# Performance work log

Measured on AMD Instinct MI355X. Metric: run time of the kernel, lower is better.

## Reference

```python
import jax, jax.numpy as jnp
import numpy as np

NUM_HEADS = 16
NUM_KV_HEADS = 4
ROPE_BASE = 10000.0
TRAIN_SEQ_LEN = 2048


def _rms_norm(x):
    eps = jnp.asarray(jnp.finfo(x.dtype).eps, x.dtype)
    return x * jax.lax.rsqrt(jnp.mean(x * x, axis=-1, keepdims=True) + eps)


def _rope_cos_sin(seq_len, head_dim, dtype):
    # seq_len <= TRAIN_SEQ_LEN -> no NTK rescaling, matches Rotary buffer path
    half = head_dim // 2
    inv_freq = 1.0 / (ROPE_BASE ** (jnp.arange(0, head_dim, 2, dtype=jnp.float32) / head_dim))
    t = jnp.arange(seq_len, dtype=jnp.float32)
    freqs = jnp.outer(t, inv_freq)  # [S, half]
    cos = jnp.cos(freqs)[None, :, None, :].astype(dtype)
    sin = jnp.sin(freqs)[None, :, None, :].astype(dtype)
    return cos, sin


def _apply_rotary(x, cos, sin):
    half = x.shape[-1] // 2
    x1, x2 = x[..., :half], x[..., half:]
    return jnp.concatenate([x1 * cos + x2 * sin, -x1 * sin + x2 * cos], axis=-1)


def setup_inputs() -> dict:
    key = jax.random.key(0)
    ks = jax.random.split(key, 5)
    B, S, D = 2, 2048, 2048
    kv_dim = NUM_KV_HEADS * (D // NUM_HEADS)
    sw = 0.02
    return {
        "x": jax.random.normal(ks[0], (B, S, D), jnp.float32),
        "Wq": jax.random.normal(ks[1], (D, D), jnp.float32) * sw,
        "Wk": jax.random.normal(ks[2], (kv_dim, D), jnp.float32) * sw,
        "Wv": jax.random.normal(ks[3], (kv_dim, D), jnp.float32) * sw,
        "Wproj": jax.random.normal(ks[4], (D, D), jnp.float32) * sw,
        "q_gain": jnp.ones((NUM_HEADS,), jnp.float32),
    }


def reference(x, Wq, Wk, Wv, Wproj, q_gain):
    B, S, D = x.shape
    H, Hkv = NUM_HEADS, NUM_KV_HEADS
    hd = D // H
    r = H // Hkv

    q = (x @ Wq.T).reshape(B, S, H, hd)
    k = (x @ Wk.T).reshape(B, S, Hkv, hd)
    v = (x @ Wv.T).reshape(B, S, Hkv, hd)

    q = _rms_norm(q)
    k = _rms_norm(k)

    cos, sin = _rope_cos_sin(S, hd, q.dtype)
    q = _apply_rotary(q, cos, sin)
    k = _apply_rotary(k, cos, sin)
    q = q * q_gain.astype(q.dtype)[None, None, :, None]

    # GQA: repeat kv heads (repeat_interleave along head dim)
    k = jnp.repeat(k, r, axis=2)  # [B,S,H,hd]
    v = jnp.repeat(v, r, axis=2)

    scale = 1.0 / jnp.sqrt(jnp.asarray(hd, q.dtype))
    scores = jnp.einsum("bqhd,bkhd->bhqk", q, k) * scale
    causal = jnp.tril(jnp.ones((S, S), dtype=bool))
    scores = jnp.where(causal[None, None], scores, jnp.asarray(-jnp.inf, scores.dtype))
    attn = jax.nn.softmax(scores, axis=-1)
    y = jnp.einsum("bhqk,bkhd->bqhd", attn, v)

    return y.reshape(B, S, D) @ Wproj.T
```

## Files before the change

### kernel.cpp

```cpp
#include <hip/hip_runtime.h>

#define D_MODEL 2048
#define SEQ 2048
#define BATCH 2
#define NH 16
#define NKV 4
#define HD 128
#define KVD (NKV * HD)
#define QKVN (D_MODEL + 2 * KVD)
#define MROWS (BATCH * SEQ)

typedef __attribute__((ext_vector_type(8))) short short8;
typedef __attribute__((ext_vector_type(4))) float f32x4;

__device__ __forceinline__ unsigned short f2bf(float f) {
    union { float f; unsigned int u; } v; v.f = f;
    unsigned int r = (v.u + 0x7FFFu + ((v.u >> 16) & 1u)) >> 16;
    return (unsigned short)r;
}

__device__ __forceinline__ unsigned short f2bf_pos(float f) {
    union { float f; unsigned int u; } v; v.f = f;
    return (unsigned short)((v.u + 0x8000u) >> 16);
}

__device__ __forceinline__ float bf2f(unsigned short u) {
    union { float f; unsigned int i; } v; v.i = ((unsigned int)u) << 16;
    return v.f;
}

__device__ __forceinline__ void async16(const void* g, void* l) {
    __builtin_amdgcn_global_load_lds((const __attribute__((address_space(1))) void*)g,
                                     (__attribute__((address_space(3))) void*)l, 16, 0, 0);
}

__global__ __launch_bounds__(256) void cast_all(const float* __restrict__ x,
                                                const float* __restrict__ wq,
                                                const float* __restrict__ wk,
                                                const float* __restrict__ wv,
                                                const float* __restrict__ wp,
                                                unsigned short* __restrict__ xb,
                                                unsigned short* __restrict__ wqkv,
                                                unsigned short* __restrict__ wpb) {
    int i = blockIdx.x * 256 + threadIdx.x;
    const float4* s; ushort4* d; int j;
    if (i < 2097152)      { s = (const float4*)x;  d = (ushort4*)xb;             j = i; }
    else if (i < 3145728) { s = (const float4*)wq; d = (ushort4*)wqkv;           j = i - 2097152; }
    else if (i < 3407872) { s = (const float4*)wk; d = (ushort4*)wqkv + 1048576; j = i - 3145728; }
    else if (i < 3670016) { s = (const float4*)wv; d = (ushort4*)wqkv + 1310720; j = i - 3407872; }
    else                  { s = (const float4*)wp; d = (ushort4*)wpb;            j = i - 3670016; }
    float4 v = s[j];
    ushort4 o;
    o.x = f2bf(v.x); o.y = f2bf(v.y); o.z = f2bf(v.z); o.w = f2bf(v.w);
    d[j] = o;
}

template <bool BF16OUT>
__global__ __launch_bounds__(256) void gemm_bt(const unsigned short* __restrict__ A,
                                               const unsigned short* __restrict__ W,
                                               void* __restrict__ Cv, int M, int N, int K) {
    __shared__ unsigned short As[128 * 32];
    __shared__ unsigned short Bs[128 * 32];
    const int tid  = threadIdx.x;
    const int lane = tid & 63;
    const int wave = tid >> 6;
    const int qm   = lane & 15;
    const int quad = lane >> 4;
    const int m0 = blockIdx.y * 128;
    const int n0 = blockIdx.x * 128;
    const int wm = (wave >> 1) * 64;
    const int wn = (wave & 1) * 64;

    f32x4 acc[4][4];
#pragma unroll
    for (int i = 0; i < 4; i++)
#pragma unroll
        for (int j = 0; j < 4; j++) acc[i][j] = (f32x4){0.f, 0.f, 0.f, 0.f};

    const int r1 = tid >> 2;
    const int c1 = (((tid & 3) ^ ((r1 >> 1) & 3)) * 8);
    const unsigned short* Ag = A + (size_t)(m0 + r1) * K + c1;
    const unsigned short* Wg = W + (size_t)(n0 + r1) * K + c1;
    unsigned short* AsW = &As[wave * 512];
    unsigned short* BsW = &Bs[wave * 512];
    const int swq = ((qm >> 1) & 3) * 8;

    for (int kt = 0; kt < K; kt += 32) {
        async16(Ag,                  AsW);
        async16(Ag + (size_t)64 * K, AsW + 2048);
        async16(Wg,                  BsW);
        async16(Wg + (size_t)64 * K, BsW + 2048);
        Ag += 32; Wg += 32;
        __syncthreads();
        short8 af[4], bfr[4];
#pragma unroll
        for (int mi = 0; mi < 4; mi++)
            af[mi] = *(const short8*)&As[(wm + mi * 16 + qm) * 32 + (quad * 8 ^ swq)];
#pragma unroll
        for (int ni = 0; ni < 4; ni++)
            bfr[ni] = *(const short8*)&Bs[(wn + ni * 16 + qm) * 32 + (quad * 8 ^ swq)];
#pragma unroll
        for (int mi = 0; mi < 4; mi++)
#pragma unroll
            for (int ni = 0; ni < 4; ni++)
                acc[mi][ni] = __builtin_amdgcn_mfma_f32_16x16x32_bf16(af[mi], bfr[ni], acc[mi][ni], 0, 0, 0);
        __syncthreads();
    }
#pragma unroll
    for (int mi = 0; mi < 4; mi++) {
#pragma unroll
        for (int r = 0; r < 4; r++) {
            int row = m0 + wm + mi * 16 + quad * 4 + r;
            if (BF16OUT) {
                unsigned short* Crow = (unsigned short*)Cv + (size_t)row * N + n0 + wn + qm;
#pragma unroll
                for (int ni = 0; ni < 4; ni++) Crow[ni * 16] = f2bf(acc[mi][ni][r]);
            } else {
                float* Crow = (float*)Cv + (size_t)row * N + n0 + wn + qm;
#pragma unroll
                for (int ni = 0; ni < 4; ni++) Crow[ni * 16] = acc[mi][ni][r];
            }
        }
    }
}

__global__ __launch_bounds__(256) void postproc(const unsigned short* __restrict__ qkvb,
                                                const float* __restrict__ gain,
                                                unsigned short* __restrict__ qb,
                                                unsigned short* __restrict__ kb) {
    const int m = blockIdx.x;
    const int b = m >> 11;
    const int s = m & 2047;
    const int wave = threadIdx.x >> 6;
    const int lane = threadIdx.x & 63;
    const unsigned short* row = qkvb + (size_t)m * QKVN;
    float inv_freq = __builtin_amdgcn_exp2f(-(float)lane * 0.20761871f);
    float ang = (float)s * inv_freq;
    float sn, cs;
    sincosf(ang, &sn, &cs);
    const float scale = 0.12751744f;
    for (int u = wave; u < 20; u += 4) {
        int off = (u < 16) ? (u * HD) : (D_MODEL + (u - 16) * HD);
        float x1 = bf2f(row[off + lane]);
        float x2 = bf2f(row[off + 64 + lane]);
        float ss = x1 * x1 + x2 * x2;
        ss += __shfl_xor(ss, 1);  ss += __shfl_xor(ss, 2);  ss += __shfl_xor(ss, 4);
        ss += __shfl_xor(ss, 8);  ss += __shfl_xor(ss, 16); ss += __shfl_xor(ss, 32);
        float rs = rsqrtf(ss * (1.0f / 128.0f) + 1.1920929e-07f);
        float a1 = x1 * rs, a2 = x2 * rs;
        float o1 = a1 * cs + a2 * sn;
        float o2 = -a1 * sn + a2 * cs;
        if (u < 16) {
            float g = gain[u] * scale;
            o1 *= g; o2 *= g;
            size_t base = ((size_t)(b * NH + u) * SEQ + s) * HD;
            qb[base + lane] = f2bf(o1);
            qb[base + 64 + lane] = f2bf(o2);
        } else {
            size_t base = ((size_t)(b * NKV + (u - 16)) * SEQ + s) * HD;
            kb[base + lane] = f2bf(o1);
            kb[base + 64 + lane] = f2bf(o2);
        }
    }
}

__global__ __launch_bounds__(256) void vtrans(const unsigned short* __restrict__ qkvb,
                                              unsigned short* __restrict__ vt) {
    __shared__ unsigned short tile[64][68];
    int idx = blockIdx.x;
    int st = idx & 31;
    int dt = (idx >> 5) & 1;
    int hk = (idx >> 6) & 3;
    int b  = idx >> 8;
    int t  = threadIdx.x;
    int cr = t >> 4;
    int cc = (t & 15) * 4;
#pragma unroll
    for (int j = 0; j < 4; j++) {
        int row = j * 16 + cr;
        const unsigned short* src = qkvb + (size_t)(b * SEQ + st * 64 + row) * QKVN
                                  + (D_MODEL + KVD) + hk * HD + dt * 64 + cc;
        *(ushort4*)&tile[row][cc] = *(const ushort4*)src;
    }
    __syncthreads();
#pragma unroll
    for (int j = 0; j < 4; j++) {
        int drow = j * 16 + cr;
        ushort4 ov;
        ov.x = tile[cc + 0][drow];
        ov.y = tile[cc + 1][drow];
        ov.z = tile[cc + 2][drow];
        ov.w = tile[cc + 3][drow];
        *(ushort4*)(vt + (size_t)((b * NKV + hk) * HD + dt * 64 + drow) * SEQ + st * 64 + cc) = ov;
    }
}

__global__ __launch_bounds__(256, 4) void attn(const unsigned short* __restrict__ qb,
                                               const unsigned short* __restrict__ kb,
                                               const unsigned short* __restrict__ vt,
                                               const float* __restrict__ gain,
                                               unsigned short* __restrict__ y) {
    __shared__ unsigned short Ks[4096];
    __shared__ unsigned short Vs[4096];
    __shared__ unsigned short plds[4][640];
    const int tid  = threadIdx.x;
    const int lane = tid & 63;
    const int wave = tid >> 6;
    const int bh   = blockIdx.x & 31;
    const int g  = blockIdx.x >> 5;
    const int gg = g & 7;
    const int gs = g >> 3;
    const int qt64 = (gs == 0) ? gg : (gs == 1) ? (31 - gg) : (gs == 2) ? (8 + gg) : (23 - gg);
    const int h = bh & 15;
    const int b = bh >> 4;
    const int qm   = lane & 15;
    const int quad = lane >> 4;
    const int q0    = qt64 * 64;
    const int qrow0 = q0 + wave * 16;
    const float M = 17.0f * fabsf(gain[h]);

    const unsigned short* Qp = qb + (((size_t)(b * NH + h)) * SEQ + qrow0) * HD;
    const unsigned short* Kp = kb + ((size_t)(b * NKV + (h >> 2))) * SEQ * HD;
    const unsigned short* Vp = vt + ((size_t)(b * NKV + (h >> 2))) * HD * SEQ;

    short8 qf[4];
#pragma unroll
    for (int c = 0; c < 4; c++)
        qf[c] = *(const short8*)(Qp + qm * HD + c * 32 + quad * 8);

    f32x4 o[8];
#pragma unroll
    for (int t = 0; t < 8; t++) o[t] = (f32x4){0.f, 0.f, 0.f, 0.f};
    float lr[4] = {0.f, 0.f, 0.f, 0.f};

    const int sr  = (tid & 127) >> 2;
    const int skc = ((tid & 3) ^ ((sr >> 1) & 3)) * 8;
    const unsigned short* KsA = Kp + sr * HD + (tid >> 7) * 32 + skc;
    const int vd  = tid >> 2;
    const int svc = ((tid & 3) ^ ((vd >> 1) & 3)) * 8;
    const unsigned short* VsA = Vp + (size_t)vd * SEQ + svc;
    char* KsB = (char*)Ks + wave * 1024;
    char* VsB = (char*)Vs + wave * 1024;
    unsigned short* P = &plds[wave][0];
    const int swq = ((qm >> 1) & 3) * 8;

    const int kvend = q0 + 64;
    for (int kv0 = 0; kv0 < kvend; kv0 += 32) {
        async16(KsA,            KsB);
        async16(KsA + 64,       KsB + 4096);
        async16(VsA,            VsB);
        async16(VsA + 64 * SEQ, VsB + 4096);
        KsA += 32 * HD;
        VsA += 32;
        __syncthreads();
        if (kv0 <= qrow0 + 15) {
            f32x4 s0 = (f32x4){0.f, 0.f, 0.f, 0.f};
            f32x4 s1 = (f32x4){0.f, 0.f, 0.f, 0.f};
#pragma unroll
            for (int c = 0; c < 4; c++) {
                short8 k0 = *(const short8*)&Ks[c * 1024 + qm * 32 + (quad * 8 ^ swq)];
                short8 k1 = *(const short8*)&Ks[c * 1024 + (16 + qm) * 32 + (quad * 8 ^ swq)];
                s0 = __builtin_amdgcn_mfma_f32_16x16x32_bf16(qf[c], k0, s0, 0, 0, 0);
                s1 = __builtin_amdgcn_mfma_f32_16x16x32_bf16(qf[c], k1, s1, 0, 0, 0);
            }
            if (kv0 + 31 > qrow0) {
#pragma unroll
                for (int r = 0; r < 4; r++) {
                    int qg = qrow0 + quad * 4 + r;
                    if (kv0 + qm > qg)      s0[r] = -3.0e38f;
                    if (kv0 + 16 + qm > qg) s1[r] = -3.0e38f;
                }
            }
            float p0[4], p1[4];
#pragma unroll
            for (int r = 0; r < 4; r++) {
                p0[r] = __builtin_amdgcn_exp2f(s0[r] - M);
                p1[r] = __builtin_amdgcn_exp2f(s1[r] - M);
                lr[r] += p0[r] + p1[r];
            }
#pragma unroll
            for (int r = 0; r < 4; r++) {
                P[(quad * 4 + r) * 40 + qm]      = f2bf_pos(p0[r]);
                P[(quad * 4 + r) * 40 + 16 + qm] = f2bf_pos(p1[r]);
            }
            short8 pa = *(const short8*)&P[qm * 40 + quad * 8];
#pragma unroll
            for (int t = 0; t < 8; t++) {
                short8 vf = *(const short8*)&Vs[(t * 16 + qm) * 32 + (quad * 8 ^ swq)];
                o[t] = __builtin_amdgcn_mfma_f32_16x16x32_bf16(pa, vf, o[t], 0, 0, 0);
            }
        }
        __syncthreads();
    }
    float rl[4];
#pragma unroll
    for (int r = 0; r < 4; r++) {
        float l = lr[r];
        l += __shfl_xor(l, 1);
        l += __shfl_xor(l, 2);
        l += __shfl_xor(l, 4);
        l += __shfl_xor(l, 8);
        rl[r] = 1.0f / l;
    }
#pragma unroll
    for (int t = 0; t < 8; t++) {
#pragma unroll
        for (int r = 0; r < 4; r++) {
            size_t row = (size_t)(b * SEQ + qrow0 + quad * 4 + r);
            y[row * D_MODEL + h * HD + t * 16 + qm] = f2bf(o[t][r] * rl[r]);
        }
    }
}

extern "C" void kernel_launch(void* const* d_in, const int* in_sizes, int n_in,
                              void* d_out, int out_size, void* d_ws, size_t ws_size,
                              hipStream_t stream) {
    const float* x  = (const float*)d_in[0];
    const float* Wq = (const float*)d_in[1];
    const float* Wk = (const float*)d_in[2];
    const float* Wv = (const float*)d_in[3];
    const float* Wp = (const float*)d_in[4];
    const float* qg = (const float*)d_in[5];

    char* ws = (char*)d_ws;
    unsigned short* xb   = (unsigned short*)(ws + 0);
    unsigned short* wqkv = (unsigned short*)(ws + 16777216);
    unsigned short* wp   = (unsigned short*)(ws + 29360128);
    unsigned short* qkvb = (unsigned short*)(ws + 37748736);
    unsigned short* qbuf = (unsigned short*)(ws + 88080384);
    unsigned short* kbuf = (unsigned short*)(ws + 104857600);
    unsigned short* vtb  = (unsigned short*)(ws + 109051904);
    unsigned short* y    = xb;

    cast_all<<<18432, 256, 0, stream>>>(x, Wq, Wk, Wv, Wp, xb, wqkv, wp);

    gemm_bt<true><<<dim3(24, 32), 256, 0, stream>>>(xb, wqkv, qkvb, MROWS, QKVN, D_MODEL);
    postproc<<<MROWS, 256, 0, stream>>>(qkvb, qg, qbuf, kbuf);
    vtrans<<<512, 256, 0, stream>>>(qkvb, vtb);
    attn<<<1024, 256, 0, stream>>>(qbuf, kbuf, vtb, qg, y);
    gemm_bt<false><<<dim3(16, 32), 256, 0, stream>>>(y, wp, (float*)d_out, MROWS, D_MODEL, D_MODEL);
}
```

Baseline: 319.0 us.

## Fuse QKV GEMM epilogue with RMSNorm/RoPE and V transpose; widen attention KV tile

Result: faster. 298.5 us (-6.4%).

```diff
diff --git a/kernel.cpp b/kernel.cpp
--- a/kernel.cpp
+++ b/kernel.cpp
@@ -55,10 +55,122 @@
     d[j] = o;
 }
 
-template <bool BF16OUT>
+__global__ __launch_bounds__(256) void gemm_qkv(const unsigned short* __restrict__ A,
+                                                const unsigned short* __restrict__ W,
+                                                const float* __restrict__ gain,
+                                                unsigned short* __restrict__ qbuf,
+                                                unsigned short* __restrict__ kbuf,
+                                                unsigned short* __restrict__ vtb) {
+    __shared__ unsigned short smem[128 * 137];
+    unsigned short* As = smem;
+    unsigned short* Bs = smem + 4096;
+    unsigned short* tile = smem;
+    const int K = D_MODEL;
+    const int tid  = threadIdx.x;
+    const int lane = tid & 63;
+    const int wave = tid >> 6;
+    const int qm   = lane & 15;
+    const int quad = lane >> 4;
+    const int m0 = blockIdx.y * 128;
+    const int bx = blockIdx.x;
+    const int n0 = bx * 128;
+    const int wm = (wave >> 1) * 64;
+    const int wn = (wave & 1) * 64;
+
+    f32x4 acc[4][4];
+#pragma unroll
+    for (int i = 0; i < 4; i++)
+#pragma unroll
+        for (int j = 0; j < 4; j++) acc[i][j] = (f32x4){0.f, 0.f, 0.f, 0.f};
+
+    const int r1 = tid >> 2;
+    const int c1 = (((tid & 3) ^ ((r1 >> 1) & 3)) * 8);
+    const unsigned short* Ag = A + (size_t)(m0 + r1) * K + c1;
+    const unsigned short* Wg = W + (size_t)(n0 + r1) * K + c1;
+    unsigned short* AsW = &As[wave * 512];
+    unsigned short* BsW = &Bs[wave * 512];
+    const int swq = ((qm >> 1) & 3) * 8;
+
+    for (int kt = 0; kt < K; kt += 32) {
+        async16(Ag,                  AsW);
+        async16(Ag + (size_t)64 * K, AsW + 2048);
+        async16(Wg,                  BsW);
+        async16(Wg + (size_t)64 * K, BsW + 2048);
+        Ag += 32; Wg += 32;
+        __syncthreads();
+        short8 af[4], bfr[4];
+#pragma unroll
+        for (int mi = 0; mi < 4; mi++)
+            af[mi] = *(const short8*)&As[(wm + mi * 16 + qm) * 32 + (quad * 8 ^ swq)];
+#pragma unroll
+        for (int ni = 0; ni < 4; ni++)
+            bfr[ni] = *(const short8*)&Bs[(wn + ni * 16 + qm) * 32 + (quad * 8 ^ swq)];
+#pragma unroll
+        for (int mi = 0; mi < 4; mi++)
+#pragma unroll
+            for (int ni = 0; ni < 4; ni++)
+                acc[mi][ni] = __builtin_amdgcn_mfma_f32_16x16x32_bf16(af[mi], bfr[ni], acc[mi][ni], 0, 0, 0);
+        __syncthreads();
+    }
+
+#pragma unroll
+    for (int mi = 0; mi < 4; mi++)
+#pragma unroll
+        for (int r = 0; r < 4; r++) {
+            int row = wm + mi * 16 + quad * 4 + r;
+#pragma unroll
+            for (int ni = 0; ni < 4; ni++)
+                tile[row * 137 + wn + ni * 16 + qm] = f2bf(acc[mi][ni][r]);
+        }
+    __syncthreads();
+
+    const int s_base = m0 & 2047;
+    const int bb = m0 >> 11;
+    if (bx < 20) {
+        const bool isq = bx < 16;
+        const float g = isq ? gain[bx] * 0.12751744f : 1.0f;
+        unsigned short* dst = isq
+            ? qbuf + ((size_t)(bb * NH + bx) * SEQ + s_base) * HD
+            : kbuf + ((size_t)(bb * NKV + (bx - 16)) * SEQ + s_base) * HD;
+        const float inv_freq = __builtin_amdgcn_exp2f(-(float)lane * 0.20761871f);
+        for (int rr = 0; rr < 32; rr++) {
+            int row = wave * 32 + rr;
+            float x1 = bf2f(tile[row * 137 + lane]);
+            float x2 = bf2f(tile[row * 137 + 64 + lane]);
+            float ss = x1 * x1 + x2 * x2;
+            ss += __shfl_xor(ss, 1);  ss += __shfl_xor(ss, 2);  ss += __shfl_xor(ss, 4);
+            ss += __shfl_xor(ss, 8);  ss += __shfl_xor(ss, 16); ss += __shfl_xor(ss, 32);
+            float rs = rsqrtf(ss * (1.0f / 128.0f) + 1.1920929e-07f);
+            float ang = (float)(s_base + row) * inv_freq;
+            float sn, cs;
+            sincosf(ang, &sn, &cs);
+            float a1 = x1 * rs, a2 = x2 * rs;
+            float o1 = (a1 * cs + a2 * sn) * g;
+            float o2 = (a2 * cs - a1 * sn) * g;
+            dst[(size_t)row * HD + lane]      = f2bf(o1);
+            dst[(size_t)row * HD + 64 + lane] = f2bf(o2);
+        }
+    } else {
+        const int hk = bx - 20;
+        unsigned short* dst = vtb + ((size_t)(bb * NKV + hk) * HD) * SEQ + s_base;
+        const int sc = (tid & 31) * 4;
+        const int d0 = tid >> 5;
+#pragma unroll
+        for (int i = 0; i < 16; i++) {
+            int d = d0 + 8 * i;
+            ushort4 ov;
+            ov.x = tile[(sc + 0) * 137 + d];
+            ov.y = tile[(sc + 1) * 137 + d];
+            ov.z = tile[(sc + 2) * 137 + d];
+            ov.w = tile[(sc + 3) * 137 + d];
+            *(ushort4*)(dst + (size_t)d * SEQ + sc) = ov;
+        }
+    }
+}
+
 __global__ __launch_bounds__(256) void gemm_bt(const unsigned short* __restrict__ A,
                                                const unsigned short* __restrict__ W,
-                                               void* __restrict__ Cv, int M, int N, int K) {
+                                               float* __restrict__ C, int M, int N, int K) {
     __shared__ unsigned short As[128 * 32];
     __shared__ unsigned short Bs[128 * 32];
     const int tid  = threadIdx.x;
@@ -111,87 +223,10 @@
 #pragma unroll
         for (int r = 0; r < 4; r++) {
             int row = m0 + wm + mi * 16 + quad * 4 + r;
-            if (BF16OUT) {
-                unsigned short* Crow = (unsigned short*)Cv + (size_t)row * N + n0 + wn + qm;
-#pragma unroll
-                for (int ni = 0; ni < 4; ni++) Crow[ni * 16] = f2bf(acc[mi][ni][r]);
-            } else {
-                float* Crow = (float*)Cv + (size_t)row * N + n0 + wn + qm;
-#pragma unroll
-                for (int ni = 0; ni < 4; ni++) Crow[ni * 16] = acc[mi][ni][r];
-            }
-        }
-    }
-}
-
-__global__ __launch_bounds__(256) void postproc(const unsigned short* __restrict__ qkvb,
-                                                const float* __restrict__ gain,
-                                                unsigned short* __restrict__ qb,
-                                                unsigned short* __restrict__ kb) {
-    const int m = blockIdx.x;
-    const int b = m >> 11;
-    const int s = m & 2047;
-    const int wave = threadIdx.x >> 6;
-    const int lane = threadIdx.x & 63;
-    const unsigned short* row = qkvb + (size_t)m * QKVN;
-    float inv_freq = __builtin_amdgcn_exp2f(-(float)lane * 0.20761871f);
-    float ang = (float)s * inv_freq;
-    float sn, cs;
-    sincosf(ang, &sn, &cs);
-    const float scale = 0.12751744f;
-    for (int u = wave; u < 20; u += 4) {
-        int off = (u < 16) ? (u * HD) : (D_MODEL + (u - 16) * HD);
-        float x1 = bf2f(row[off + lane]);
-        float x2 = bf2f(row[off + 64 + lane]);
-        float ss = x1 * x1 + x2 * x2;
-        ss += __shfl_xor(ss, 1);  ss += __shfl_xor(ss, 2);  ss += __shfl_xor(ss, 4);
-        ss += __shfl_xor(ss, 8);  ss += __shfl_xor(ss, 16); ss += __shfl_xor(ss, 32);
-        float rs = rsqrtf(ss * (1.0f / 128.0f) + 1.1920929e-07f);
-        float a1 = x1 * rs, a2 = x2 * rs;
-        float o1 = a1 * cs + a2 * sn;
-        float o2 = -a1 * sn + a2 * cs;
-        if (u < 16) {
-            float g = gain[u] * scale;
-            o1 *= g; o2 *= g;
-            size_t base = ((size_t)(b * NH + u) * SEQ + s) * HD;
-            qb[base + lane] = f2bf(o1);
-            qb[base + 64 + lane] = f2bf(o2);
-        } else {
-            size_t base = ((size_t)(b * NKV + (u - 16)) * SEQ + s) * HD;
-            kb[base + lane] = f2bf(o1);
-            kb[base + 64 + lane] = f2bf(o2);
-        }
-    }
-}
-
-__global__ __launch_bounds__(256) void vtrans(const unsigned short* __restrict__ qkvb,
-                                              unsigned short* __restrict__ vt) {
-    __shared__ unsigned short tile[64][68];
-    int idx = blockIdx.x;
-    int st = idx & 31;
-    int dt = (idx >> 5) & 1;
-    int hk = (idx >> 6) & 3;
-    int b  = idx >> 8;
-    int t  = threadIdx.x;
-    int cr = t >> 4;
-    int cc = (t & 15) * 4;
-#pragma unroll
-    for (int j = 0; j < 4; j++) {
-        int row = j * 16 + cr;
-        const unsigned short* src = qkvb + (size_t)(b * SEQ + st * 64 + row) * QKVN
-                                  + (D_MODEL + KVD) + hk * HD + dt * 64 + cc;
-        *(ushort4*)&tile[row][cc] = *(const ushort4*)src;
-    }
-    __syncthreads();
-#pragma unroll
-    for (int j = 0; j < 4; j++) {
-        int drow = j * 16 + cr;
-        ushort4 ov;
-        ov.x = tile[cc + 0][drow];
-        ov.y = tile[cc + 1][drow];
-        ov.z = tile[cc + 2][drow];
-        ov.w = tile[cc + 3][drow];
-        *(ushort4*)(vt + (size_t)((b * NKV + hk) * HD + dt * 64 + drow) * SEQ + st * 64 + cc) = ov;
+            float* Crow = C + (size_t)row * N + n0 + wn + qm;
+#pragma unroll
+            for (int ni = 0; ni < 4; ni++) Crow[ni * 16] = acc[mi][ni][r];
+        }
     }
 }
 
@@ -200,16 +235,16 @@
                                                const unsigned short* __restrict__ vt,
                                                const float* __restrict__ gain,
                                                unsigned short* __restrict__ y) {
-    __shared__ unsigned short Ks[4096];
-    __shared__ unsigned short Vs[4096];
-    __shared__ unsigned short plds[4][640];
+    __shared__ unsigned short Ks[8192];
+    __shared__ unsigned short Vs[8192];
+    __shared__ unsigned short plds[4][1024];
     const int tid  = threadIdx.x;
     const int lane = tid & 63;
     const int wave = tid >> 6;
     const int bh   = blockIdx.x & 31;
-    const int g  = blockIdx.x >> 5;
-    const int gg = g & 7;
-    const int gs = g >> 3;
+    const int g4   = blockIdx.x >> 5;
+    const int gg = g4 & 7;
+    const int gs = g4 >> 3;
     const int qt64 = (gs == 0) ? gg : (gs == 1) ? (31 - gg) : (gs == 2) ? (8 + gg) : (23 - gg);
     const int h = bh & 15;
     const int b = bh >> 4;
@@ -233,61 +268,68 @@
     for (int t = 0; t < 8; t++) o[t] = (f32x4){0.f, 0.f, 0.f, 0.f};
     float lr[4] = {0.f, 0.f, 0.f, 0.f};
 
-    const int sr  = (tid & 127) >> 2;
-    const int skc = ((tid & 3) ^ ((sr >> 1) & 3)) * 8;
-    const unsigned short* KsA = Kp + sr * HD + (tid >> 7) * 32 + skc;
-    const int vd  = tid >> 2;
-    const int svc = ((tid & 3) ^ ((vd >> 1) & 3)) * 8;
-    const unsigned short* VsA = Vp + (size_t)vd * SEQ + svc;
+    const unsigned short* KsA = Kp + (size_t)(tid >> 4) * HD + (((tid & 15) ^ (tid >> 4)) & 15) * 8;
+    const unsigned short* VsA = Vp + (size_t)(tid >> 3) * SEQ + (((tid & 7) ^ ((tid >> 3) & 7)) * 8);
     char* KsB = (char*)Ks + wave * 1024;
     char* VsB = (char*)Vs + wave * 1024;
     unsigned short* P = &plds[wave][0];
-    const int swq = ((qm >> 1) & 3) * 8;
 
     const int kvend = q0 + 64;
-    for (int kv0 = 0; kv0 < kvend; kv0 += 32) {
-        async16(KsA,            KsB);
-        async16(KsA + 64,       KsB + 4096);
-        async16(VsA,            VsB);
-        async16(VsA + 64 * SEQ, VsB + 4096);
-        KsA += 32 * HD;
-        VsA += 32;
-        __syncthreads();
-        if (kv0 <= qrow0 + 15) {
-            f32x4 s0 = (f32x4){0.f, 0.f, 0.f, 0.f};
-            f32x4 s1 = (f32x4){0.f, 0.f, 0.f, 0.f};
-#pragma unroll
-            for (int c = 0; c < 4; c++) {
-                short8 k0 = *(const short8*)&Ks[c * 1024 + qm * 32 + (quad * 8 ^ swq)];
-                short8 k1 = *(const short8*)&Ks[c * 1024 + (16 + qm) * 32 + (quad * 8 ^ swq)];
-                s0 = __builtin_amdgcn_mfma_f32_16x16x32_bf16(qf[c], k0, s0, 0, 0, 0);
-                s1 = __builtin_amdgcn_mfma_f32_16x16x32_bf16(qf[c], k1, s1, 0, 0, 0);
+    for (int kv0 = 0; kv0 < kvend; kv0 += 64) {
+#pragma unroll
+        for (int i = 0; i < 4; i++) {
+            async16(KsA + (size_t)(16 * i) * HD,  KsB + i * 4096);
+            async16(VsA + (size_t)(32 * i) * SEQ, VsB + i * 4096);
+        }
+        KsA += (size_t)64 * HD;
+        VsA += 64;
+        __syncthreads();
+
+        f32x4 s[4];
+#pragma unroll
+        for (int g = 0; g < 4; g++) s[g] = (f32x4){0.f, 0.f, 0.f, 0.f};
+#pragma unroll
+        for (int c = 0; c < 4; c++) {
+#pragma unroll
+            for (int g = 0; g < 4; g++) {
+                short8 kf = *(const short8*)&Ks[(g * 16 + qm) * 128 + (((c * 4 + quad) ^ qm) * 8)];
+                s[g] = __builtin_amdgcn_mfma_f32_16x16x32_bf16(qf[c], kf, s[g], 0, 0, 0);
             }
-            if (kv0 + 31 > qrow0) {
+        }
+        if (kv0 + 63 > qrow0) {
+#pragma unroll
+            for (int g = 0; g < 4; g++)
 #pragma unroll
                 for (int r = 0; r < 4; r++) {
                     int qg = qrow0 + quad * 4 + r;
-                    if (kv0 + qm > qg)      s0[r] = -3.0e38f;
-                    if (kv0 + 16 + qm > qg) s1[r] = -3.0e38f;
+                    if (kv0 + g * 16 + qm > qg) s[g][r] = -3.0e38f;
                 }
+        }
+        float p[4][4];
+#pragma unroll
+        for (int g = 0; g < 4; g++)
+#pragma unroll
+            for (int r = 0; r < 4; r++) {
+                p[g][r] = __builtin_amdgcn_exp2f(s[g][r] - M);
+                lr[r] += p[g][r];
             }
-            float p0[4], p1[4];
+#pragma unroll
+        for (int g = 0; g < 4; g++)
 #pragma unroll
             for (int r = 0; r < 4; r++) {
-                p0[r] = __builtin_amdgcn_exp2f(s0[r] - M);
-                p1[r] = __builtin_amdgcn_exp2f(s1[r] - M);
-                lr[r] += p0[r] + p1[r];
+                int rowp = quad * 4 + r;
+                P[rowp * 64 + (((g * 2 + (qm >> 3)) ^ (rowp & 7)) * 8) + (qm & 7)] = f2bf_pos(p[g][r]);
             }
-#pragma unroll
-            for (int r = 0; r < 4; r++) {
-                P[(quad * 4 + r) * 40 + qm]      = f2bf_pos(p0[r]);
-                P[(quad * 4 + r) * 40 + 16 + qm] = f2bf_pos(p1[r]);
-            }
-            short8 pa = *(const short8*)&P[qm * 40 + quad * 8];
-#pragma unroll
-            for (int t = 0; t < 8; t++) {
-                short8 vf = *(const short8*)&Vs[(t * 16 + qm) * 32 + (quad * 8 ^ swq)];
-                o[t] = __builtin_amdgcn_mfma_f32_16x16x32_bf16(pa, vf, o[t], 0, 0, 0);
+        short8 pa[2];
+#pragma unroll
+        for (int ka = 0; ka < 2; ka++)
+            pa[ka] = *(const short8*)&P[qm * 64 + (((ka * 4 + quad) ^ (qm & 7)) * 8)];
+#pragma unroll
+        for (int t = 0; t < 8; t++) {
+#pragma unroll
+            for (int ka = 0; ka < 2; ka++) {
+                short8 vf = *(const short8*)&Vs[(t * 16 + qm) * 64 + (((ka * 4 + quad) ^ (qm & 7)) * 8)];
+                o[t] = __builtin_amdgcn_mfma_f32_16x16x32_bf16(pa[ka], vf, o[t], 0, 0, 0);
             }
         }
         __syncthreads();
@@ -326,17 +368,13 @@
     unsigned short* xb   = (unsigned short*)(ws + 0);
     unsigned short* wqkv = (unsigned short*)(ws + 16777216);
     unsigned short* wp   = (unsigned short*)(ws + 29360128);
-    unsigned short* qkvb = (unsigned short*)(ws + 37748736);
-    unsigned short* qbuf = (unsigned short*)(ws + 88080384);
-    unsigned short* kbuf = (unsigned short*)(ws + 104857600);
-    unsigned short* vtb  = (unsigned short*)(ws + 109051904);
+    unsigned short* qbuf = (unsigned short*)(ws + 37748736);
+    unsigned short* kbuf = (unsigned short*)(ws + 54525952);
+    unsigned short* vtb  = (unsigned short*)(ws + 58720256);
     unsigned short* y    = xb;
 
     cast_all<<<18432, 256, 0, stream>>>(x, Wq, Wk, Wv, Wp, xb, wqkv, wp);
-
-    gemm_bt<true><<<dim3(24, 32), 256, 0, stream>>>(xb, wqkv, qkvb, MROWS, QKVN, D_MODEL);
-    postproc<<<MROWS, 256, 0, stream>>>(qkvb, qg, qbuf, kbuf);
-    vtrans<<<512, 256, 0, stream>>>(qkvb, vtb);
+    gemm_qkv<<<dim3(24, 32), 256, 0, stream>>>(xb, wqkv, qg, qbuf, kbuf, vtb);
     attn<<<1024, 256, 0, stream>>>(qbuf, kbuf, vtb, qg, y);
-    gemm_bt<false><<<dim3(16, 32), 256, 0, stream>>>(y, wp, (float*)d_out, MROWS, D_MODEL, D_MODEL);
-}
+    gemm_bt<<<dim3(16, 32), 256, 0, stream>>>(y, wp, (float*)d_out, MROWS, D_MODEL, D_MODEL);
+}
```
